# Kernel optimization log

Hardware: AMD Instinct MI355X
Metric: run time of the kernel (lower is better)

## Reference

```python
import jax, jax.numpy as jnp
import numpy as np

E = 1024      # hidden_dim
H = 16        # num_heads
D = E // H    # head_dim
S = 2048      # seq_len == max_seq_len
B = 4


def setup_inputs() -> dict:
    key = jax.random.key(0)
    ks = jax.random.split(key, 6)
    x = jax.random.normal(ks[0], (B, S, E), dtype=jnp.float32)
    # nn.MultiheadAttention params: packed in_proj (3E, E) + bias, out_proj (E, E) + bias
    in_proj_w = jax.random.normal(ks[1], (3 * E, E), dtype=jnp.float32) * (1.0 / np.sqrt(E))
    in_proj_b = jnp.zeros((3 * E,), dtype=jnp.float32)
    out_proj_w = jax.random.normal(ks[2], (E, E), dtype=jnp.float32) * (1.0 / np.sqrt(E))
    out_proj_b = jnp.zeros((E,), dtype=jnp.float32)
    rel_pos = jax.random.normal(ks[3], (S, S), dtype=jnp.float32) * 0.02
    return {"x": x, "in_proj_w": in_proj_w, "in_proj_b": in_proj_b,
            "out_proj_w": out_proj_w, "out_proj_b": out_proj_b, "rel_pos": rel_pos}


def reference(x, in_proj_w, in_proj_b, out_proj_w, out_proj_b, rel_pos):
    b, s, _ = x.shape
    # packed QKV projection: y = x @ W^T + b (torch Linear convention)
    qkv = x @ in_proj_w.T + in_proj_b                  # [B,S,3E]
    q, k, v = jnp.split(qkv, 3, axis=-1)               # each [B,S,E]
    q = q.reshape(b, s, H, D).transpose(0, 2, 1, 3)    # [B,H,S,D]
    k = k.reshape(b, s, H, D).transpose(0, 2, 1, 3)
    v = v.reshape(b, s, H, D).transpose(0, 2, 1, 3)
    scale = 1.0 / np.sqrt(D)
    scores = jnp.einsum('bhqd,bhkd->bhqk', q * scale, k)
    scores = scores + rel_pos[:s, :s]                  # additive learnable rel-pos bias
    attn = jax.nn.softmax(scores, axis=-1)
    out = jnp.einsum('bhqk,bhkd->bhqd', attn, v)       # [B,H,S,D]
    out = out.transpose(0, 2, 1, 3).reshape(b, s, E)
    return out @ out_proj_w.T + out_proj_b
```

## Files before the change

### kernel.cpp

```cpp
#include <hip/hip_runtime.h>
#include <cstddef>
#include <cstdint>

constexpr int B = 4, S = 2048, E = 1024, H = 16, D = 64;
constexpr int M_ROWS = B * S;
constexpr float LOG2E = 1.4426950408889634f;

typedef __bf16 bf16x8 __attribute__((ext_vector_type(8)));
typedef float  f32x4  __attribute__((ext_vector_type(4)));

__device__ __forceinline__ unsigned short f2bf(float x) {
    union { float f; uint32_t u; } v; v.f = x;
    uint32_t r = v.u + 0x7fff + ((v.u >> 16) & 1);
    return (unsigned short)(r >> 16);
}
__device__ __forceinline__ unsigned short f2bf_fast(float x) {
    return __builtin_bit_cast(unsigned short, (__bf16)x);
}
__device__ __forceinline__ void gld_lds16(const unsigned short* g, unsigned short* l) {
    __builtin_amdgcn_global_load_lds(
        (const __attribute__((address_space(1))) void*)g,
        (__attribute__((address_space(3))) void*)l, 16, 0, 0);
}
__device__ __forceinline__ void drain_publish() {
    asm volatile("s_waitcnt vmcnt(0)" ::: "memory");
    __builtin_amdgcn_sched_barrier(0);
    __syncthreads();
}

__global__ __launch_bounds__(256)
void cvt_bf16(const float* __restrict__ x,  unsigned short* __restrict__ xb,
              const float* __restrict__ w1, unsigned short* __restrict__ w1b,
              const float* __restrict__ w2, unsigned short* __restrict__ w2b)
{
    const int bid = blockIdx.x;
    const float* s; unsigned short* d; size_t idx;
    if (bid < 4096)      { s = x;  d = xb;  idx = (size_t)bid * 256 + threadIdx.x; }
    else if (bid < 5632) { s = w1; d = w1b; idx = (size_t)(bid - 4096) * 256 + threadIdx.x; }
    else                 { s = w2; d = w2b; idx = (size_t)(bid - 5632) * 256 + threadIdx.x; }
    const float4* s4 = (const float4*)s;
    float4 v0 = s4[idx * 2], v1 = s4[idx * 2 + 1];
    float f[8] = { v0.x, v0.y, v0.z, v0.w, v1.x, v1.y, v1.z, v1.w };
    unsigned short hh[8];
    #pragma unroll
    for (int j = 0; j < 8; ++j) hh[j] = f2bf(f[j]);
    ((int4*)d)[idx] = *(const int4*)hh;
}

template<int MODE, int KD>
__global__ __launch_bounds__(256)
void gemm_bf16(const unsigned short* __restrict__ A, const unsigned short* __restrict__ W,
               const float* __restrict__ bias, float* __restrict__ C,
               unsigned short* __restrict__ qd, unsigned short* __restrict__ kd,
               unsigned short* __restrict__ vd, int M, int N)
{
    __shared__ __align__(16) unsigned short lds[2][2][128 * 32];

    const int t    = threadIdx.x;
    const int wid  = t >> 6, lane = t & 63;
    const int l16  = lane & 15, lg = lane >> 4;
    const int wr   = wid >> 1, wc = wid & 1;
    const int m0   = blockIdx.y * 128;
    const int n0   = blockIdx.x * 128;

    const unsigned short* ga = A + (size_t)m0 * KD;
    const unsigned short* gw = W + (size_t)n0 * KD;

    int srow[2], soff[2];
    #pragma unroll
    for (int half = 0; half < 2; ++half) {
        int c   = half * 256 + t;
        int row = c >> 2, cc = c & 3;
        srow[half] = row;
        soff[half] = (cc ^ ((row >> 1) & 3)) * 8;
    }

    f32x4 acc[4][4];
    #pragma unroll
    for (int mi = 0; mi < 4; ++mi)
        #pragma unroll
        for (int ni = 0; ni < 4; ++ni) acc[mi][ni] = (f32x4){0.f, 0.f, 0.f, 0.f};

    auto stage = [&](int k0, int buf) {
        #pragma unroll
        for (int half = 0; half < 2; ++half) {
            unsigned short* la = &lds[buf][0][(half * 256 + wid * 64) * 8];
            unsigned short* lw = &lds[buf][1][(half * 256 + wid * 64) * 8];
            gld_lds16(ga + (size_t)srow[half] * KD + k0 + soff[half], la);
            gld_lds16(gw + (size_t)srow[half] * KD + k0 + soff[half], lw);
        }
    };

    stage(0, 0);
    drain_publish();

    constexpr int NIT = KD / 32;
    for (int it = 0; it < NIT; ++it) {
        const int cur = it & 1;
        if (it + 1 < NIT) stage((it + 1) * 32, cur ^ 1);

        bf16x8 a[4], b[4];
        #pragma unroll
        for (int mi = 0; mi < 4; ++mi) {
            int arow = wr * 64 + mi * 16 + l16;
            a[mi] = *(const bf16x8*)&lds[cur][0][arow * 32 + ((lg ^ ((arow >> 1) & 3)) << 3)];
        }
        #pragma unroll
        for (int ni = 0; ni < 4; ++ni) {
            int brow = wc * 64 + ni * 16 + l16;
            b[ni] = *(const bf16x8*)&lds[cur][1][brow * 32 + ((lg ^ ((brow >> 1) & 3)) << 3)];
        }
        #pragma unroll
        for (int mi = 0; mi < 4; ++mi)
            #pragma unroll
            for (int ni = 0; ni < 4; ++ni)
                acc[mi][ni] = __builtin_amdgcn_mfma_f32_16x16x32_bf16(a[mi], b[ni], acc[mi][ni], 0, 0, 0);

        drain_publish();
    }

    const int colblk = n0 + wc * 64;
    if constexpr (MODE == 0) {
        #pragma unroll
        for (int mi = 0; mi < 4; ++mi)
            #pragma unroll
            for (int r = 0; r < 4; ++r) {
                int row = m0 + wr * 64 + mi * 16 + lg * 4 + r;
                #pragma unroll
                for (int ni = 0; ni < 4; ++ni) {
                    int col = colblk + ni * 16 + l16;
                    C[(size_t)row * N + col] = acc[mi][ni][r] + bias[col];
                }
            }
    } else {
        const int which = colblk >> 10;
        const int e0    = colblk & (E - 1);
        const int h_    = e0 >> 6;
        const int rowg0 = m0 + wr * 64;
        const int b_    = rowg0 >> 11;
        const int s0g   = rowg0 & (S - 1);

        if (which < 2) {
            unsigned short* dst = (which == 0) ? qd : kd;
            const float osc = (which == 0) ? 0.125f * LOG2E : 1.0f;
            #pragma unroll
            for (int mi = 0; mi < 4; ++mi)
                #pragma unroll
                for (int r = 0; r < 4; ++r) {
                    int s_ = s0g + mi * 16 + lg * 4 + r;
                    #pragma unroll
                    for (int ni = 0; ni < 4; ++ni) {
                        int col = colblk + ni * 16 + l16;
                        int d_  = col & 63;
                        dst[(((size_t)(b_ * H + h_)) * S + s_) * D + d_] =
                            f2bf((acc[mi][ni][r] + bias[col]) * osc);
                    }
                }
        } else {
            unsigned short* et = &lds[0][0][0] + wid * 2048;
            #pragma unroll
            for (int p = 0; p < 2; ++p) {
                #pragma unroll
                for (int nj = 0; nj < 2; ++nj) {
                    int ni   = p * 2 + nj;
                    int dloc = nj * 16 + l16;
                    float bv = bias[colblk + ni * 16 + l16];
                    #pragma unroll
                    for (int mi = 0; mi < 4; ++mi)
                        #pragma unroll
                        for (int r = 0; r < 4; ++r) {
                            int s = mi * 16 + lg * 4 + r;
                            et[dloc * 64 + (((s >> 3) ^ (dloc & 7)) << 3) + (s & 7)] =
                                f2bf(acc[mi][ni][r] + bv);
                        }
                }
                #pragma unroll
                for (int it = 0; it < 4; ++it) {
                    int c  = it * 64 + lane;
                    int dd = c >> 3, j8 = c & 7;
                    int4 vv = *(const int4*)&et[dd * 64 + ((j8 ^ (dd & 7)) << 3)];
                    *(int4*)&vd[(((size_t)(b_ * H + h_)) * D + p * 32 + dd) * S + s0g + j8 * 8] = vv;
                }
            }
        }
    }
}

__global__ __launch_bounds__(256)
void attn_mfma(const unsigned short* __restrict__ Qb,
               const unsigned short* __restrict__ Kb,
               const unsigned short* __restrict__ Vtb,
               const float* __restrict__ rel,
               unsigned short* __restrict__ AOb)
{
    __shared__ unsigned short lds_k[4096];
    __shared__ unsigned short lds_v[4096];
    __shared__ unsigned short lds_p[4][1024];

    const int t    = threadIdx.x;
    const int wid  = t >> 6, lane = t & 63;
    const int l16  = lane & 15, lg = lane >> 4;
    const int bh   = blockIdx.y;
    const int q0   = blockIdx.x * 64;
    const int b_   = bh >> 4, h_ = bh & 15;

    const size_t qkoff = (size_t)bh * S * D;
    const size_t vtoff = (size_t)bh * D * S;

    bf16x8 qf[2];
    {
        const unsigned short* qrow = Qb + qkoff + (size_t)(q0 + wid * 16 + l16) * D;
        qf[0] = *(const bf16x8*)(qrow + lg * 8);
        qf[1] = *(const bf16x8*)(qrow + 32 + lg * 8);
    }

    float l_run[4] = {0.f, 0.f, 0.f, 0.f};
    f32x4 o[4];
    #pragma unroll
    for (int dt = 0; dt < 4; ++dt) o[dt] = (f32x4){0.f, 0.f, 0.f, 0.f};

    for (int k0 = 0; k0 < S; k0 += 64) {
        __syncthreads();
        #pragma unroll
        for (int i = 0; i < 2; ++i) {
            int c   = wid * 128 + i * 64 + lane;
            int row = c >> 3, cc = c & 7;
            int sc  = cc ^ (row & 7);
            const unsigned short* gk = Kb  + qkoff + (size_t)(k0 + row) * D + sc * 8;
            *(int4*)&lds_k[c * 8] = *(const int4*)gk;
            const unsigned short* gv = Vtb + vtoff + (size_t)row * S + k0 + sc * 8;
            *(int4*)&lds_v[c * 8] = *(const int4*)gv;
        }
        __syncthreads();

        f32x4 acc[4];
        #pragma unroll
        for (int kt = 0; kt < 4; ++kt) acc[kt] = (f32x4){0.f, 0.f, 0.f, 0.f};
        #pragma unroll
        for (int f = 0; f < 2; ++f) {
            #pragma unroll
            for (int kt = 0; kt < 4; ++kt) {
                int key   = kt * 16 + l16;
                int chunk = (f * 4 + lg) ^ (key & 7);
                bf16x8 kf = *(const bf16x8*)&lds_k[key * 64 + chunk * 8];
                acc[kt] = __builtin_amdgcn_mfma_f32_16x16x32_bf16(qf[f], kf, acc[kt], 0, 0, 0);
            }
        }

        const float* relbase = rel + (size_t)(q0 + wid * 16) * S + k0;
        unsigned short* pw = &lds_p[wid][0];
        #pragma unroll
        for (int kt = 0; kt < 4; ++kt) {
            #pragma unroll
            for (int r = 0; r < 4; ++r) {
                float relv = relbase[(size_t)(lg * 4 + r) * S + kt * 16 + l16];
                float pv = __builtin_amdgcn_exp2f(fmaf(relv, LOG2E, acc[kt][r]));
                l_run[r] += pv;
                int qr = lg * 4 + r;
                int k  = kt * 16 + l16;
                pw[qr * 64 + (((k >> 3) ^ (qr & 7)) << 3) + (k & 7)] = f2bf_fast(pv);
            }
        }

        #pragma unroll
        for (int f = 0; f < 2; ++f) {
            int pchunk = (f * 4 + lg) ^ (l16 & 7);
            bf16x8 pf = *(const bf16x8*)&pw[l16 * 64 + pchunk * 8];
            #pragma unroll
            for (int dt = 0; dt < 4; ++dt) {
                int d      = dt * 16 + l16;
                int vchunk = (f * 4 + lg) ^ (d & 7);
                bf16x8 vf  = *(const bf16x8*)&lds_v[d * 64 + vchunk * 8];
                o[dt] = __builtin_amdgcn_mfma_f32_16x16x32_bf16(pf, vf, o[dt], 0, 0, 0);
            }
        }
    }

    #pragma unroll
    for (int r = 0; r < 4; ++r) {
        float v = l_run[r];
        v += __shfl_xor(v, 1);
        v += __shfl_xor(v, 2);
        v += __shfl_xor(v, 4);
        v += __shfl_xor(v, 8);
        l_run[r] = v;
    }

    #pragma unroll
    for (int r = 0; r < 4; ++r) {
        float inv = 1.f / l_run[r];
        int qr = q0 + wid * 16 + lg * 4 + r;
        size_t base = ((size_t)b_ * S + qr) * E + h_ * 64;
        #pragma unroll
        for (int dt = 0; dt < 4; ++dt)
            AOb[base + dt * 16 + l16] = f2bf(o[dt][r] * inv);
    }
}

extern "C" void kernel_launch(void* const* d_in, const int* in_sizes, int n_in,
                              void* d_out, int out_size, void* d_ws, size_t ws_size,
                              hipStream_t stream)
{
    const float* x   = (const float*)d_in[0];
    const float* w1  = (const float*)d_in[1];
    const float* b1  = (const float*)d_in[2];
    const float* w2  = (const float*)d_in[3];
    const float* b2  = (const float*)d_in[4];
    const float* rel = (const float*)d_in[5];
    float* out = (float*)d_out;

    unsigned short* p = (unsigned short*)d_ws;
    unsigned short* xb  = p;  p += (size_t)M_ROWS * E;
    unsigned short* w1b = p;  p += (size_t)3 * E * E;
    unsigned short* w2b = p;  p += (size_t)E * E;
    unsigned short* qb  = p;  p += (size_t)B * H * S * D;
    unsigned short* kb  = p;  p += (size_t)B * H * S * D;
    unsigned short* vb  = p;
    unsigned short* AOb = xb;

    cvt_bf16<<<dim3(6144), dim3(256), 0, stream>>>(x, xb, w1, w1b, w2, w2b);

    dim3 g1(3 * E / 128, M_ROWS / 128);
    gemm_bf16<1, 1024><<<g1, dim3(256), 0, stream>>>(xb, w1b, b1, nullptr,
                                                     qb, kb, vb, M_ROWS, 3 * E);

    dim3 g2(S / 64, B * H);
    attn_mfma<<<g2, dim3(256), 0, stream>>>(qb, kb, vb, rel, AOb);

    dim3 g3(E / 128, M_ROWS / 128);
    gemm_bf16<0, 1024><<<g3, dim3(256), 0, stream>>>(AOb, w2b, b2, out,
                                                     nullptr, nullptr, nullptr, M_ROWS, E);
}
```

Baseline: 255.3 us.

## Convert rel-pos bias to bf16 and stage it through LDS in attention

The fp32 relative-position bias is now converted to bf16 in the existing conversion kernel, and the attention kernel loads each 64x64 bias tile cooperatively into LDS with coalesced 16-byte loads instead of strided per-lane fp32 global reads. The LDS P buffer is reused: bias values are read from a slot and overwritten with the probability in place. This halves bias bytes and improves access coalescing, at the cost of an extra conversion pass and bf16 rounding of the bias.

```diff
diff --git a/kernel.cpp b/kernel.cpp
--- a/kernel.cpp
+++ b/kernel.cpp
@@ -14,6 +14,9 @@
     uint32_t r = v.u + 0x7fff + ((v.u >> 16) & 1);
     return (unsigned short)(r >> 16);
 }
+__device__ __forceinline__ float bf2f(unsigned short h) {
+    union { uint32_t u; float f; } v; v.u = (uint32_t)h << 16; return v.f;
+}
 __device__ __forceinline__ unsigned short f2bf_fast(float x) {
     return __builtin_bit_cast(unsigned short, (__bf16)x);
 }
@@ -31,13 +34,15 @@
 __global__ __launch_bounds__(256)
 void cvt_bf16(const float* __restrict__ x,  unsigned short* __restrict__ xb,
               const float* __restrict__ w1, unsigned short* __restrict__ w1b,
-              const float* __restrict__ w2, unsigned short* __restrict__ w2b)
+              const float* __restrict__ w2, unsigned short* __restrict__ w2b,
+              const float* __restrict__ rl, unsigned short* __restrict__ rlb)
 {
     const int bid = blockIdx.x;
     const float* s; unsigned short* d; size_t idx;
     if (bid < 4096)      { s = x;  d = xb;  idx = (size_t)bid * 256 + threadIdx.x; }
     else if (bid < 5632) { s = w1; d = w1b; idx = (size_t)(bid - 4096) * 256 + threadIdx.x; }
-    else                 { s = w2; d = w2b; idx = (size_t)(bid - 5632) * 256 + threadIdx.x; }
+    else if (bid < 6144) { s = w2; d = w2b; idx = (size_t)(bid - 5632) * 256 + threadIdx.x; }
+    else                 { s = rl; d = rlb; idx = (size_t)(bid - 6144) * 256 + threadIdx.x; }
     const float4* s4 = (const float4*)s;
     float4 v0 = s4[idx * 2], v1 = s4[idx * 2 + 1];
     float f[8] = { v0.x, v0.y, v0.z, v0.w, v1.x, v1.y, v1.z, v1.w };
@@ -190,12 +195,12 @@
 void attn_mfma(const unsigned short* __restrict__ Qb,
                const unsigned short* __restrict__ Kb,
                const unsigned short* __restrict__ Vtb,
-               const float* __restrict__ rel,
+               const unsigned short* __restrict__ Rlb,
                unsigned short* __restrict__ AOb)
 {
     __shared__ unsigned short lds_k[4096];
     __shared__ unsigned short lds_v[4096];
-    __shared__ unsigned short lds_p[4][1024];
+    __shared__ unsigned short lds_pr[4096];
 
     const int t    = threadIdx.x;
     const int wid  = t >> 6, lane = t & 63;
@@ -226,10 +231,12 @@
             int c   = wid * 128 + i * 64 + lane;
             int row = c >> 3, cc = c & 7;
             int sc  = cc ^ (row & 7);
-            const unsigned short* gk = Kb  + qkoff + (size_t)(k0 + row) * D + sc * 8;
-            *(int4*)&lds_k[c * 8] = *(const int4*)gk;
-            const unsigned short* gv = Vtb + vtoff + (size_t)row * S + k0 + sc * 8;
-            *(int4*)&lds_v[c * 8] = *(const int4*)gv;
+            *(int4*)&lds_k[c * 8] =
+                *(const int4*)(Kb + qkoff + (size_t)(k0 + row) * D + sc * 8);
+            *(int4*)&lds_v[c * 8] =
+                *(const int4*)(Vtb + vtoff + (size_t)row * S + k0 + sc * 8);
+            *(int4*)&lds_pr[c * 8] =
+                *(const int4*)(Rlb + (size_t)(q0 + row) * S + k0 + sc * 8);
         }
         __syncthreads();
 
@@ -247,18 +254,18 @@
             }
         }
 
-        const float* relbase = rel + (size_t)(q0 + wid * 16) * S + k0;
-        unsigned short* pw = &lds_p[wid][0];
+        unsigned short* pw = &lds_pr[wid * 1024];
         #pragma unroll
         for (int kt = 0; kt < 4; ++kt) {
             #pragma unroll
             for (int r = 0; r < 4; ++r) {
-                float relv = relbase[(size_t)(lg * 4 + r) * S + kt * 16 + l16];
+                int qr   = lg * 4 + r;
+                int k    = kt * 16 + l16;
+                int slot = qr * 64 + (((k >> 3) ^ (qr & 7)) << 3) + (k & 7);
+                float relv = bf2f(pw[slot]);
                 float pv = __builtin_amdgcn_exp2f(fmaf(relv, LOG2E, acc[kt][r]));
                 l_run[r] += pv;
-                int qr = lg * 4 + r;
-                int k  = kt * 16 + l16;
-                pw[qr * 64 + (((k >> 3) ^ (qr & 7)) << 3) + (k & 7)] = f2bf_fast(pv);
+                pw[slot] = f2bf_fast(pv);
             }
         }
 
@@ -315,17 +322,18 @@
     unsigned short* w2b = p;  p += (size_t)E * E;
     unsigned short* qb  = p;  p += (size_t)B * H * S * D;
     unsigned short* kb  = p;  p += (size_t)B * H * S * D;
-    unsigned short* vb  = p;
+    unsigned short* vb  = p;  p += (size_t)B * H * S * D;
+    unsigned short* rlb = p;
     unsigned short* AOb = xb;
 
-    cvt_bf16<<<dim3(6144), dim3(256), 0, stream>>>(x, xb, w1, w1b, w2, w2b);
+    cvt_bf16<<<dim3(8192), dim3(256), 0, stream>>>(x, xb, w1, w1b, w2, w2b, rel, rlb);
 
     dim3 g1(3 * E / 128, M_ROWS / 128);
     gemm_bf16<1, 1024><<<g1, dim3(256), 0, stream>>>(xb, w1b, b1, nullptr,
                                                      qb, kb, vb, M_ROWS, 3 * E);
 
     dim3 g2(S / 64, B * H);
-    attn_mfma<<<g2, dim3(256), 0, stream>>>(qb, kb, vb, rel, AOb);
+    attn_mfma<<<g2, dim3(256), 0, stream>>>(qb, kb, vb, rlb, AOb);
 
     dim3 g3(E / 128, M_ROWS / 128);
     gemm_bf16<0, 1024><<<g3, dim3(256), 0, stream>>>(AOb, w2b, b2, out,
```

Measured after the change: 265.1 us. +3.8%, slower.
